# Performance work log

Measured on AMD Instinct MI355X. Metric: run time of the kernel, lower is better.

The kernel has to match this reference:

```python
import jax, jax.numpy as jnp
import numpy as np

B, K, T, H = 64, 49, 512, 512  # batch, regions, timesteps, hidden_size
A = 49                          # attention bottleneck dim (hard-coded in module)


def setup_inputs() -> dict:
    key = jax.random.key(0)
    ks = jax.random.split(key, 7)
    s = 1.0 / np.sqrt(H)
    return {
        "V":   jax.random.normal(ks[0], (B, K, H), jnp.float32),
        "h_t": jax.random.normal(ks[1], (B, T, H), jnp.float32),
        "s_t": jax.random.normal(ks[2], (B, T, H), jnp.float32),
        "Wv":  jax.random.normal(ks[3], (A, H), jnp.float32) * s,
        "Wg":  jax.random.normal(ks[4], (A, H), jnp.float32) * s,
        "Ws":  jax.random.normal(ks[5], (A, H), jnp.float32) * s,
        "Wh":  jax.random.normal(ks[6], (1, A), jnp.float32) * (1.0 / np.sqrt(A)),
    }


def reference(V, h_t, s_t, Wv, Wg, Ws, Wh):
    # Dropout is identity (eval mode). torch.nn.Linear: y = x @ W.T
    wh = Wh[0]                                     # [A]
    cv = jnp.einsum('bkh,ah->bka', V, Wv)          # [B,K,A]
    gh = jnp.einsum('bth,ah->bta', h_t, Wg)        # [B,T,A]
    content_v = cv[:, None, :, :] + gh[:, :, None, :]      # [B,T,K,A]
    z_t = jnp.einsum('btka,a->btk', jnp.tanh(content_v), wh)  # [B,T,K]
    alpha_t = jax.nn.softmax(z_t, axis=-1)         # softmax over K regions
    c_t = jnp.einsum('btk,bkh->bth', alpha_t, V)   # [B,T,H]

    content_s = jnp.einsum('bth,ah->bta', s_t, Ws) + gh       # [B,T,A]
    z_ext = jnp.einsum('bta,a->bt', jnp.tanh(content_s), wh)  # [B,T]
    extended = jnp.concatenate([z_t, z_ext[:, :, None]], axis=2)  # [B,T,K+1]
    alpha_hat = jax.nn.softmax(extended, axis=-1)
    beta_t = alpha_hat[:, :, -1:]                  # [B,T,1] sentinel gate

    c_hat_t = beta_t * s_t + (1.0 - beta_t) * c_t  # [B,T,H]
    return c_hat_t, alpha_t, beta_t
```

## Files before the change

kernel.cpp:

```cpp
#include <hip/hip_runtime.h>
#include <hip/hip_bf16.h>
#include <cstdint>
#include <cstddef>

#define NB 64
#define NK 49
#define NT 512
#define NH 512
#define NA 49

typedef __attribute__((ext_vector_type(8))) short bf16x8;
typedef __attribute__((ext_vector_type(4))) float f32x4;

__device__ __forceinline__ float fast_exp(float x) {
    return __builtin_amdgcn_exp2f(x * 1.4426950408889634f);
}
__device__ __forceinline__ float fast_tanh(float x) {
    float e = __builtin_amdgcn_exp2f(x * 2.8853900817779268f);
    return 1.0f - 2.0f * __builtin_amdgcn_rcpf(e + 1.0f);
}
__device__ __forceinline__ short bf16rn(float x) {
    unsigned b = __builtin_bit_cast(unsigned, x);
    unsigned r = b + 0x7FFFu + ((b >> 16) & 1u);
    return (short)(r >> 16);
}
__device__ __forceinline__ void split_hi_lo(float x, short& hi, short& lo) {
    unsigned b = __builtin_bit_cast(unsigned, x);
    unsigned hb = b & 0xFFFF0000u;
    hi = (short)(hb >> 16);
    lo = bf16rn(x - __builtin_bit_cast(float, hb));
}
__device__ __forceinline__ bf16x8 cvt8(float4 x0, float4 x1) {
    bf16x8 a;
    a[0] = bf16rn(x0.x); a[1] = bf16rn(x0.y); a[2] = bf16rn(x0.z); a[3] = bf16rn(x0.w);
    a[4] = bf16rn(x1.x); a[5] = bf16rn(x1.y); a[6] = bf16rn(x1.z); a[7] = bf16rn(x1.w);
    return a;
}

__global__ __launch_bounds__(256, 4) void kprew(
        const float* __restrict__ Wg, const float* __restrict__ Ws,
        const float* __restrict__ Wv, short* __restrict__ WB) {
    const int job = blockIdx.x >> 3, slice = blockIdx.x & 7;
    const float* W = (job == 0) ? Wg : (job == 1 ? Ws : Wv);
    short* dst = WB + (size_t)job * 65536;
    const int end = (slice + 1) * 8192;
    for (int idx = slice * 8192 + threadIdx.x; idx < end; idx += 256) {
        int e    = idx & 7;
        int lane = (idx >> 3) & 63;
        int ks   = (idx >> 9) & 15;
        int nt   = (idx >> 13) & 3;
        int sel  = idx >> 15;
        int a = nt * 16 + (lane & 15);
        int h = ks * 32 + (lane >> 4) * 8 + e;
        float x = (a < NA) ? W[a * NH + h] : 0.0f;
        short hi, lo; split_hi_lo(x, hi, lo);
        dst[idx] = sel ? lo : hi;
    }
}

__global__ __launch_bounds__(256, 4) void kprev(
        const float* __restrict__ V, const short* __restrict__ WB,
        short* __restrict__ VB, float* __restrict__ cv) {
    const int bid = blockIdx.x;
    if (bid < 512) {
        __shared__ float vl[NK * 64];
        const int b  = bid >> 3;
        const int sl = bid & 7;
        const int h0 = sl * 64;
        const float* Vb = V + (size_t)b * (NK * NH);
        for (int idx = threadIdx.x; idx < NK * 64; idx += 256) {
            int k = idx >> 6, c = idx & 63;
            vl[idx] = Vb[(size_t)k * NH + h0 + c];
        }
        __syncthreads();
        short* dst = VB + (size_t)b * 32768;
        for (int idx = threadIdx.x; idx < 4096; idx += 256) {
            int e    = idx & 7;
            int lane = (idx >> 3) & 63;
            int ks   = (idx >> 9) & 1;
            int ntl  = idx >> 10;
            int k = ks * 32 + (lane >> 4) * 8 + e;
            int c = ntl * 16 + (lane & 15);
            float x = (k < NK) ? vl[k * 64 + c] : 0.0f;
            dst[((size_t)(sl * 4 + ntl) * 2 + ks) * 512 + lane * 8 + e] = bf16rn(x);
        }
    } else {
        const int tid  = threadIdx.x;
        const int lane = tid & 63;
        const int w    = tid >> 6;
        const int m0   = (bid - 512) * 64 + w * 16;
        const int r    = lane & 15;
        const int g    = lane >> 4;

        const float* arow = V + (size_t)(m0 + r) * NH + g * 8;
        const bf16x8* wbv = (const bf16x8*)(WB + 2 * 65536);

        f32x4 acc0 = {0.f, 0.f, 0.f, 0.f};
        f32x4 acc1 = acc0, acc2 = acc0, acc3 = acc0;

        #pragma unroll 2
        for (int ks = 0; ks < 16; ++ks) {
            float4 x0 = *(const float4*)(arow + ks * 32);
            float4 x1 = *(const float4*)(arow + ks * 32 + 4);
            bf16x8 bh0 = wbv[(0 * 16 + ks) * 64 + lane];
            bf16x8 bh1 = wbv[(1 * 16 + ks) * 64 + lane];
            bf16x8 bh2 = wbv[(2 * 16 + ks) * 64 + lane];
            bf16x8 bh3 = wbv[(3 * 16 + ks) * 64 + lane];
            bf16x8 bl0 = wbv[(4 * 16 + ks) * 64 + lane];
            bf16x8 bl1 = wbv[(5 * 16 + ks) * 64 + lane];
            bf16x8 bl2 = wbv[(6 * 16 + ks) * 64 + lane];
            bf16x8 bl3 = wbv[(7 * 16 + ks) * 64 + lane];

            bf16x8 ahi, alo;
            {
                const float xs[8] = {x0.x, x0.y, x0.z, x0.w, x1.x, x1.y, x1.z, x1.w};
                #pragma unroll
                for (int e = 0; e < 8; ++e) { short hi, lo; split_hi_lo(xs[e], hi, lo); ahi[e] = hi; alo[e] = lo; }
            }
            acc0 = __builtin_amdgcn_mfma_f32_16x16x32_bf16(ahi, bh0, acc0, 0, 0, 0);
            acc0 = __builtin_amdgcn_mfma_f32_16x16x32_bf16(alo, bh0, acc0, 0, 0, 0);
            acc0 = __builtin_amdgcn_mfma_f32_16x16x32_bf16(ahi, bl0, acc0, 0, 0, 0);
            acc1 = __builtin_amdgcn_mfma_f32_16x16x32_bf16(ahi, bh1, acc1, 0, 0, 0);
            acc1 = __builtin_amdgcn_mfma_f32_16x16x32_bf16(alo, bh1, acc1, 0, 0, 0);
            acc1 = __builtin_amdgcn_mfma_f32_16x16x32_bf16(ahi, bl1, acc1, 0, 0, 0);
            acc2 = __builtin_amdgcn_mfma_f32_16x16x32_bf16(ahi, bh2, acc2, 0, 0, 0);
            acc2 = __builtin_amdgcn_mfma_f32_16x16x32_bf16(alo, bh2, acc2, 0, 0, 0);
            acc2 = __builtin_amdgcn_mfma_f32_16x16x32_bf16(ahi, bl2, acc2, 0, 0, 0);
            acc3 = __builtin_amdgcn_mfma_f32_16x16x32_bf16(ahi, bh3, acc3, 0, 0, 0);
            acc3 = __builtin_amdgcn_mfma_f32_16x16x32_bf16(alo, bh3, acc3, 0, 0, 0);
            acc3 = __builtin_amdgcn_mfma_f32_16x16x32_bf16(ahi, bl3, acc3, 0, 0, 0);
        }

        #pragma unroll
        for (int reg = 0; reg < 4; ++reg) {
            int row = m0 + g * 4 + reg;
            float* orow = cv + (size_t)row * 52;
            orow[ 0 + r] = acc0[reg];
            orow[16 + r] = acc1[reg];
            orow[32 + r] = acc2[reg];
            if (r == 0) orow[48] = acc3[reg];
        }
    }
}

__global__ __launch_bounds__(256, 4) void kfused(
        const float* __restrict__ h_t, const float* __restrict__ s_t,
        const float* __restrict__ Wh,
        const short* __restrict__ WB, const short* __restrict__ VB,
        const float* __restrict__ cv_ws,
        float* __restrict__ out_chat, float* __restrict__ out_alpha,
        float* __restrict__ out_beta) {
    __shared__ float cvl[NK * 52];
    __shared__ float ghl[32 * 52];
    __shared__ float ssl[32 * 52];
    __shared__ float zl[32 * 50];
    __shared__ short afrag[2048];
    __shared__ float whl[52];
    __shared__ float betal[32];

    const int tid  = threadIdx.x;
    const int lane = tid & 63;
    const int w    = tid >> 6;
    const int b    = blockIdx.x >> 4;
    const int t0   = (blockIdx.x & 15) * 32;
    const int r    = lane & 15;
    const int g    = lane >> 4;

    if (tid < NA) whl[tid] = Wh[tid];

    {
        const float* cvb = cv_ws + (size_t)b * (NK * 52);
        for (int idx = tid; idx < NK * 52; idx += 256) cvl[idx] = cvb[idx];
    }

    {
        const int job = w >> 1, mtile = w & 1;
        const float* in = job ? s_t : h_t;
        const bf16x8* wb = (const bf16x8*)(WB + (size_t)job * 65536);
        const float* arow = in + (size_t)(b * NT + t0 + mtile * 16 + r) * NH + g * 8;
        f32x4 acc0 = {0.f, 0.f, 0.f, 0.f};
        f32x4 acc1 = acc0, acc2 = acc0, acc3 = acc0;
        #pragma unroll 1
        for (int kp = 0; kp < 8; ++kp) {
            const int ksa = kp * 2, ksb = kp * 2 + 1;
            float4 xa0 = *(const float4*)(arow + ksa * 32);
            float4 xa1 = *(const float4*)(arow + ksa * 32 + 4);
            float4 xb0 = *(const float4*)(arow + ksb * 32);
            float4 xb1 = *(const float4*)(arow + ksb * 32 + 4);
            bf16x8 bh0a = wb[((0 + 0) * 16 + ksa) * 64 + lane];
            bf16x8 bh1a = wb[((0 + 1) * 16 + ksa) * 64 + lane];
            bf16x8 bh2a = wb[((0 + 2) * 16 + ksa) * 64 + lane];
            bf16x8 bh3a = wb[((0 + 3) * 16 + ksa) * 64 + lane];
            bf16x8 bl0a = wb[((4 + 0) * 16 + ksa) * 64 + lane];
            bf16x8 bl1a = wb[((4 + 1) * 16 + ksa) * 64 + lane];
            bf16x8 bl2a = wb[((4 + 2) * 16 + ksa) * 64 + lane];
            bf16x8 bl3a = wb[((4 + 3) * 16 + ksa) * 64 + lane];
            bf16x8 bh0b = wb[((0 + 0) * 16 + ksb) * 64 + lane];
            bf16x8 bh1b = wb[((0 + 1) * 16 + ksb) * 64 + lane];
            bf16x8 bh2b = wb[((0 + 2) * 16 + ksb) * 64 + lane];
            bf16x8 bh3b = wb[((0 + 3) * 16 + ksb) * 64 + lane];
            bf16x8 bl0b = wb[((4 + 0) * 16 + ksb) * 64 + lane];
            bf16x8 bl1b = wb[((4 + 1) * 16 + ksb) * 64 + lane];
            bf16x8 bl2b = wb[((4 + 2) * 16 + ksb) * 64 + lane];
            bf16x8 bl3b = wb[((4 + 3) * 16 + ksb) * 64 + lane];

            bf16x8 aa = cvt8(xa0, xa1);
            acc0 = __builtin_amdgcn_mfma_f32_16x16x32_bf16(aa, bh0a, acc0, 0, 0, 0);
            acc0 = __builtin_amdgcn_mfma_f32_16x16x32_bf16(aa, bl0a, acc0, 0, 0, 0);
            acc1 = __builtin_amdgcn_mfma_f32_16x16x32_bf16(aa, bh1a, acc1, 0, 0, 0);
            acc1 = __builtin_amdgcn_mfma_f32_16x16x32_bf16(aa, bl1a, acc1, 0, 0, 0);
            acc2 = __builtin_amdgcn_mfma_f32_16x16x32_bf16(aa, bh2a, acc2, 0, 0, 0);
            acc2 = __builtin_amdgcn_mfma_f32_16x16x32_bf16(aa, bl2a, acc2, 0, 0, 0);
            acc3 = __builtin_amdgcn_mfma_f32_16x16x32_bf16(aa, bh3a, acc3, 0, 0, 0);
            acc3 = __builtin_amdgcn_mfma_f32_16x16x32_bf16(aa, bl3a, acc3, 0, 0, 0);

            bf16x8 ab = cvt8(xb0, xb1);
            acc0 = __builtin_amdgcn_mfma_f32_16x16x32_bf16(ab, bh0b, acc0, 0, 0, 0);
            acc0 = __builtin_amdgcn_mfma_f32_16x16x32_bf16(ab, bl0b, acc0, 0, 0, 0);
            acc1 = __builtin_amdgcn_mfma_f32_16x16x32_bf16(ab, bh1b, acc1, 0, 0, 0);
            acc1 = __builtin_amdgcn_mfma_f32_16x16x32_bf16(ab, bl1b, acc1, 0, 0, 0);
            acc2 = __builtin_amdgcn_mfma_f32_16x16x32_bf16(ab, bh2b, acc2, 0, 0, 0);
            acc2 = __builtin_amdgcn_mfma_f32_16x16x32_bf16(ab, bl2b, acc2, 0, 0, 0);
            acc3 = __builtin_amdgcn_mfma_f32_16x16x32_bf16(ab, bh3b, acc3, 0, 0, 0);
            acc3 = __builtin_amdgcn_mfma_f32_16x16x32_bf16(ab, bl3b, acc3, 0, 0, 0);
        }
        float* dst = (w >> 1) ? ssl : ghl;
        #pragma unroll
        for (int reg = 0; reg < 4; ++reg) {
            int m = mtile * 16 + g * 4 + reg;
            dst[m * 52 +  0 + r] = acc0[reg];
            dst[m * 52 + 16 + r] = acc1[reg];
            dst[m * 52 + 32 + r] = acc2[reg];
            if (r < 4) dst[m * 52 + 48 + r] = acc3[reg];
        }
    }
    __syncthreads();

    {
        for (int p = tid; p < 32 * NK; p += 256) {
            int t = (int)(((unsigned)p * 1338u) >> 16);
            int k = p - t * NK;
            const float* rowp = cvl + k * 52;
            const float* gp   = ghl + t * 52;
            float zx = 0.f, zy = 0.f, zz = 0.f, zw = 0.f;
            #pragma unroll
            for (int q = 0; q < 12; ++q) {
                float4 rr = *(const float4*)(rowp + q * 4);
                float4 gg = *(const float4*)(gp + q * 4);
                zx = fmaf(whl[q * 4 + 0], fast_tanh(rr.x + gg.x), zx);
                zy = fmaf(whl[q * 4 + 1], fast_tanh(rr.y + gg.y), zy);
                zz = fmaf(whl[q * 4 + 2], fast_tanh(rr.z + gg.z), zz);
                zw = fmaf(whl[q * 4 + 3], fast_tanh(rr.w + gg.w), zw);
            }
            float z = (zx + zy) + (zz + zw);
            zl[t * 50 + k] = fmaf(whl[48], fast_tanh(rowp[48] + gp[48]), z);
        }
    }
    __syncthreads();

    {
        const int trow = w * 8 + (lane >> 3);
        const int sub  = lane & 7;
        float* zr = zl + trow * 50;

        float m = -1e30f;
        for (int k = sub; k < NK; k += 8) m = fmaxf(m, zr[k]);
        m = fmaxf(m, __shfl_xor(m, 1));
        m = fmaxf(m, __shfl_xor(m, 2));
        m = fmaxf(m, __shfl_xor(m, 4));

        float S = 0.0f;
        for (int k = sub; k < NK; k += 8) S += fast_exp(zr[k] - m);
        S += __shfl_xor(S, 1);
        S += __shfl_xor(S, 2);
        S += __shfl_xor(S, 4);
        float rS = __builtin_amdgcn_rcpf(S);

        const float* sp = ssl + trow * 52;
        const float* gp = ghl + trow * 52;
        float ze = 0.0f;
        for (int a = sub; a < NA; a += 8) ze = fmaf(whl[a], fast_tanh(sp[a] + gp[a]), ze);
        ze += __shfl_xor(ze, 1);
        ze += __shfl_xor(ze, 2);
        ze += __shfl_xor(ze, 4);

        float m50  = fmaxf(m, ze);
        float eext = fast_exp(ze - m50);
        float beta = eext * __builtin_amdgcn_rcpf(S * fast_exp(m - m50) + eext);
        if (sub == 0) {
            betal[trow] = beta;
            out_beta[(size_t)b * NT + t0 + trow] = beta;
        }

        const int mt = trow >> 4, rr2 = trow & 15;
        for (int k = sub; k < 64; k += 8) {
            float a = (k < NK) ? fast_exp(zr[k] - m) * rS : 0.0f;
            if (k < NK) zr[k] = a;
            int ks = k >> 5, gg = (k & 31) >> 3;
            afrag[(((ks * 2 + mt) * 64) + gg * 16 + rr2) * 8 + sub] = bf16rn(a);
        }
    }
    __syncthreads();

    {
        float* oa = out_alpha + ((size_t)b * NT + t0) * NK;
        for (int idx = tid; idx < 32 * NK; idx += 256) {
            int t = (int)(((unsigned)idx * 1338u) >> 16);
            int k = idx - t * NK;
            oa[idx] = zl[t * 50 + k];
        }
    }

    {
        const bf16x8* af = (const bf16x8*)afrag;
        const bf16x8* vb = (const bf16x8*)(VB + (size_t)b * 32768);
        const size_t rowb = (size_t)b * NT + t0;

        bf16x8 a00 = af[(0 * 2 + 0) * 64 + lane];
        bf16x8 a01 = af[(0 * 2 + 1) * 64 + lane];
        bf16x8 a10 = af[(1 * 2 + 0) * 64 + lane];
        bf16x8 a11 = af[(1 * 2 + 1) * 64 + lane];

        #pragma unroll 2
        for (int ntl = 0; ntl < 8; ++ntl) {
            const int nt = w * 8 + ntl;
            bf16x8 b0 = vb[(nt * 2 + 0) * 64 + lane];
            bf16x8 b1 = vb[(nt * 2 + 1) * 64 + lane];
            f32x4 acc0 = {0.f, 0.f, 0.f, 0.f};
            f32x4 acc1 = acc0;
            acc0 = __builtin_amdgcn_mfma_f32_16x16x32_bf16(a00, b0, acc0, 0, 0, 0);
            acc0 = __builtin_amdgcn_mfma_f32_16x16x32_bf16(a10, b1, acc0, 0, 0, 0);
            acc1 = __builtin_amdgcn_mfma_f32_16x16x32_bf16(a01, b0, acc1, 0, 0, 0);
            acc1 = __builtin_amdgcn_mfma_f32_16x16x32_bf16(a11, b1, acc1, 0, 0, 0);

            const int h0 = nt * 16 + r;
            #pragma unroll
            for (int reg = 0; reg < 4; ++reg) {
                {
                    int tloc = g * 4 + reg;
                    float bt = betal[tloc];
                    size_t off = (rowb + tloc) * NH + h0;
                    float s = s_t[off];
                    out_chat[off] = fmaf(bt, s - acc0[reg], acc0[reg]);
                }
                {
                    int tloc = 16 + g * 4 + reg;
                    float bt = betal[tloc];
                    size_t off = (rowb + tloc) * NH + h0;
                    float s = s_t[off];
                    out_chat[off] = fmaf(bt, s - acc1[reg], acc1[reg]);
                }
            }
        }
    }
}

extern "C" void kernel_launch(void* const* d_in, const int* in_sizes, int n_in,
                              void* d_out, int out_size, void* d_ws, size_t ws_size,
                              hipStream_t stream) {
    const float* V   = (const float*)d_in[0];
    const float* h_t = (const float*)d_in[1];
    const float* s_t = (const float*)d_in[2];
    const float* Wv  = (const float*)d_in[3];
    const float* Wg  = (const float*)d_in[4];
    const float* Ws  = (const float*)d_in[5];
    const float* Wh  = (const float*)d_in[6];

    float* out = (float*)d_out;
    float* out_chat  = out;
    float* out_alpha = out + (size_t)NB * NT * NH;
    float* out_beta  = out_alpha + (size_t)NB * NT * NK;

    short* WB = (short*)d_ws;
    short* VB = WB + (size_t)3 * 65536;
    float* cv = (float*)(VB + (size_t)64 * 32768);

    kprew<<<24, 256, 0, stream>>>(Wg, Ws, Wv, WB);
    kprev<<<561, 256, 0, stream>>>(V, WB, VB, cv);
    kfused<<<NB * 16, 256, 0, stream>>>(h_t, s_t, Wh, WB, VB, cv,
                                        out_chat, out_alpha, out_beta);
}
```

Measured before the change: 95.73 us.

## Halve fused kernel tile to 16 timesteps with 128 threads, read cv from global

The fused kernel now processes 16 timesteps per block with 2 waves instead of 32 timesteps with 4 waves, which doubles the grid and shrinks shared memory. The per-batch cv tile is no longer staged in LDS. Each thread reads its cv row straight from global/L2 into registers, with the tanh-sum loop unrolled by hand. The aim is higher occupancy and less LDS staging, at the cost of more redundant weight and cv reads across the larger number of blocks.

```diff
diff --git a/kernel.cpp b/kernel.cpp
--- a/kernel.cpp
+++ b/kernel.cpp
@@ -8,6 +8,7 @@
 #define NT 512
 #define NH 512
 #define NA 49
+#define TT 16
 
 typedef __attribute__((ext_vector_type(8))) short bf16x8;
 typedef __attribute__((ext_vector_type(4))) float f32x4;
@@ -143,41 +144,34 @@
     }
 }
 
-__global__ __launch_bounds__(256, 4) void kfused(
+__global__ __launch_bounds__(128, 4) void kfused(
         const float* __restrict__ h_t, const float* __restrict__ s_t,
         const float* __restrict__ Wh,
         const short* __restrict__ WB, const short* __restrict__ VB,
         const float* __restrict__ cv_ws,
         float* __restrict__ out_chat, float* __restrict__ out_alpha,
         float* __restrict__ out_beta) {
-    __shared__ float cvl[NK * 52];
-    __shared__ float ghl[32 * 52];
-    __shared__ float ssl[32 * 52];
-    __shared__ float zl[32 * 50];
-    __shared__ short afrag[2048];
+    __shared__ float ghl[TT * 52];
+    __shared__ float ssl[TT * 52];
+    __shared__ float zl[TT * 50];
+    __shared__ short afrag[1024];
     __shared__ float whl[52];
-    __shared__ float betal[32];
+    __shared__ float betal[TT];
 
     const int tid  = threadIdx.x;
     const int lane = tid & 63;
     const int w    = tid >> 6;
-    const int b    = blockIdx.x >> 4;
-    const int t0   = (blockIdx.x & 15) * 32;
+    const int b    = blockIdx.x >> 5;
+    const int t0   = (blockIdx.x & 31) * TT;
     const int r    = lane & 15;
     const int g    = lane >> 4;
 
     if (tid < NA) whl[tid] = Wh[tid];
 
     {
-        const float* cvb = cv_ws + (size_t)b * (NK * 52);
-        for (int idx = tid; idx < NK * 52; idx += 256) cvl[idx] = cvb[idx];
-    }
-
-    {
-        const int job = w >> 1, mtile = w & 1;
-        const float* in = job ? s_t : h_t;
-        const bf16x8* wb = (const bf16x8*)(WB + (size_t)job * 65536);
-        const float* arow = in + (size_t)(b * NT + t0 + mtile * 16 + r) * NH + g * 8;
+        const float* in = w ? s_t : h_t;
+        const bf16x8* wb = (const bf16x8*)(WB + (size_t)w * 65536);
+        const float* arow = in + (size_t)(b * NT + t0 + r) * NH + g * 8;
         f32x4 acc0 = {0.f, 0.f, 0.f, 0.f};
         f32x4 acc1 = acc0, acc2 = acc0, acc3 = acc0;
         #pragma unroll 1
@@ -224,10 +218,10 @@
             acc3 = __builtin_amdgcn_mfma_f32_16x16x32_bf16(ab, bh3b, acc3, 0, 0, 0);
             acc3 = __builtin_amdgcn_mfma_f32_16x16x32_bf16(ab, bl3b, acc3, 0, 0, 0);
         }
-        float* dst = (w >> 1) ? ssl : ghl;
+        float* dst = w ? ssl : ghl;
         #pragma unroll
         for (int reg = 0; reg < 4; ++reg) {
-            int m = mtile * 16 + g * 4 + reg;
+            int m = g * 4 + reg;
             dst[m * 52 +  0 + r] = acc0[reg];
             dst[m * 52 + 16 + r] = acc1[reg];
             dst[m * 52 + 32 + r] = acc2[reg];
@@ -237,23 +231,40 @@
     __syncthreads();
 
     {
-        for (int p = tid; p < 32 * NK; p += 256) {
+        const float* cvb = cv_ws + (size_t)b * (NK * 52);
+        for (int p = tid; p < TT * NK; p += 128) {
             int t = (int)(((unsigned)p * 1338u) >> 16);
             int k = p - t * NK;
-            const float* rowp = cvl + k * 52;
+            const float* rowp = cvb + (size_t)k * 52;
             const float* gp   = ghl + t * 52;
+            float4 rr0 = *(const float4*)(rowp +  0);
+            float4 rr1 = *(const float4*)(rowp +  4);
+            float4 rr2 = *(const float4*)(rowp +  8);
+            float4 rr3 = *(const float4*)(rowp + 12);
+            float4 rr4 = *(const float4*)(rowp + 16);
+            float4 rr5 = *(const float4*)(rowp + 20);
+            float4 rr6 = *(const float4*)(rowp + 24);
+            float4 rr7 = *(const float4*)(rowp + 28);
+            float4 rr8 = *(const float4*)(rowp + 32);
+            float4 rr9 = *(const float4*)(rowp + 36);
+            float4 rrA = *(const float4*)(rowp + 40);
+            float4 rrB = *(const float4*)(rowp + 44);
+            float r48  = rowp[48];
             float zx = 0.f, zy = 0.f, zz = 0.f, zw = 0.f;
-            #pragma unroll
-            for (int q = 0; q < 12; ++q) {
-                float4 rr = *(const float4*)(rowp + q * 4);
-                float4 gg = *(const float4*)(gp + q * 4);
-                zx = fmaf(whl[q * 4 + 0], fast_tanh(rr.x + gg.x), zx);
-                zy = fmaf(whl[q * 4 + 1], fast_tanh(rr.y + gg.y), zy);
-                zz = fmaf(whl[q * 4 + 2], fast_tanh(rr.z + gg.z), zz);
-                zw = fmaf(whl[q * 4 + 3], fast_tanh(rr.w + gg.w), zw);
-            }
+            const float4* gp4 = (const float4*)gp;
+            float4 gg;
+            #define ZSTEP(RR, Q) \
+                gg = gp4[Q]; \
+                zx = fmaf(whl[(Q)*4+0], fast_tanh(RR.x + gg.x), zx); \
+                zy = fmaf(whl[(Q)*4+1], fast_tanh(RR.y + gg.y), zy); \
+                zz = fmaf(whl[(Q)*4+2], fast_tanh(RR.z + gg.z), zz); \
+                zw = fmaf(whl[(Q)*4+3], fast_tanh(RR.w + gg.w), zw);
+            ZSTEP(rr0, 0)  ZSTEP(rr1, 1)  ZSTEP(rr2, 2)  ZSTEP(rr3, 3)
+            ZSTEP(rr4, 4)  ZSTEP(rr5, 5)  ZSTEP(rr6, 6)  ZSTEP(rr7, 7)
+            ZSTEP(rr8, 8)  ZSTEP(rr9, 9)  ZSTEP(rrA,10)  ZSTEP(rrB,11)
+            #undef ZSTEP
             float z = (zx + zy) + (zz + zw);
-            zl[t * 50 + k] = fmaf(whl[48], fast_tanh(rowp[48] + gp[48]), z);
+            zl[t * 50 + k] = fmaf(whl[48], fast_tanh(r48 + gp[48]), z);
         }
     }
     __syncthreads();
@@ -292,19 +303,18 @@
             out_beta[(size_t)b * NT + t0 + trow] = beta;
         }
 
-        const int mt = trow >> 4, rr2 = trow & 15;
         for (int k = sub; k < 64; k += 8) {
             float a = (k < NK) ? fast_exp(zr[k] - m) * rS : 0.0f;
             if (k < NK) zr[k] = a;
             int ks = k >> 5, gg = (k & 31) >> 3;
-            afrag[(((ks * 2 + mt) * 64) + gg * 16 + rr2) * 8 + sub] = bf16rn(a);
+            afrag[((ks * 64) + gg * 16 + trow) * 8 + sub] = bf16rn(a);
         }
     }
     __syncthreads();
 
     {
         float* oa = out_alpha + ((size_t)b * NT + t0) * NK;
-        for (int idx = tid; idx < 32 * NK; idx += 256) {
+        for (int idx = tid; idx < TT * NK; idx += 128) {
             int t = (int)(((unsigned)idx * 1338u) >> 16);
             int k = idx - t * NK;
             oa[idx] = zl[t * 50 + k];
@@ -316,40 +326,43 @@
         const bf16x8* vb = (const bf16x8*)(VB + (size_t)b * 32768);
         const size_t rowb = (size_t)b * NT + t0;
 
-        bf16x8 a00 = af[(0 * 2 + 0) * 64 + lane];
-        bf16x8 a01 = af[(0 * 2 + 1) * 64 + lane];
-        bf16x8 a10 = af[(1 * 2 + 0) * 64 + lane];
-        bf16x8 a11 = af[(1 * 2 + 1) * 64 + lane];
+        bf16x8 a0 = af[  0 + lane];
+        bf16x8 a1 = af[ 64 + lane];
+
+        const float bt0 = betal[g * 4 + 0];
+        const float bt1 = betal[g * 4 + 1];
+        const float bt2 = betal[g * 4 + 2];
+        const float bt3 = betal[g * 4 + 3];
 
         #pragma unroll 2
-        for (int ntl = 0; ntl < 8; ++ntl) {
-            const int nt = w * 8 + ntl;
+        for (int ntl = 0; ntl < 16; ++ntl) {
+            const int nt = w * 16 + ntl;
             bf16x8 b0 = vb[(nt * 2 + 0) * 64 + lane];
             bf16x8 b1 = vb[(nt * 2 + 1) * 64 + lane];
-            f32x4 acc0 = {0.f, 0.f, 0.f, 0.f};
-            f32x4 acc1 = acc0;
-            acc0 = __builtin_amdgcn_mfma_f32_16x16x32_bf16(a00, b0, acc0, 0, 0, 0);
-            acc0 = __builtin_amdgcn_mfma_f32_16x16x32_bf16(a10, b1, acc0, 0, 0, 0);
-            acc1 = __builtin_amdgcn_mfma_f32_16x16x32_bf16(a01, b0, acc1, 0, 0, 0);
-            acc1 = __builtin_amdgcn_mfma_f32_16x16x32_bf16(a11, b1, acc1, 0, 0, 0);
+            f32x4 acc = {0.f, 0.f, 0.f, 0.f};
+            acc = __builtin_amdgcn_mfma_f32_16x16x32_bf16(a0, b0, acc, 0, 0, 0);
+            acc = __builtin_amdgcn_mfma_f32_16x16x32_bf16(a1, b1, acc, 0, 0, 0);
 
             const int h0 = nt * 16 + r;
-            #pragma unroll
-            for (int reg = 0; reg < 4; ++reg) {
-                {
-                    int tloc = g * 4 + reg;
-                    float bt = betal[tloc];
-                    size_t off = (rowb + tloc) * NH + h0;
-                    float s = s_t[off];
-                    out_chat[off] = fmaf(bt, s - acc0[reg], acc0[reg]);
-                }
-                {
-                    int tloc = 16 + g * 4 + reg;
-                    float bt = betal[tloc];
-                    size_t off = (rowb + tloc) * NH + h0;
-                    float s = s_t[off];
-                    out_chat[off] = fmaf(bt, s - acc1[reg], acc1[reg]);
-                }
+            {
+                size_t off = (rowb + g * 4 + 0) * NH + h0;
+                float s = s_t[off];
+                out_chat[off] = fmaf(bt0, s - acc[0], acc[0]);
+            }
+            {
+                size_t off = (rowb + g * 4 + 1) * NH + h0;
+                float s = s_t[off];
+                out_chat[off] = fmaf(bt1, s - acc[1], acc[1]);
+            }
+            {
+                size_t off = (rowb + g * 4 + 2) * NH + h0;
+                float s = s_t[off];
+                out_chat[off] = fmaf(bt2, s - acc[2], acc[2]);
+            }
+            {
+                size_t off = (rowb + g * 4 + 3) * NH + h0;
+                float s = s_t[off];
+                out_chat[off] = fmaf(bt3, s - acc[3], acc[3]);
             }
         }
     }
@@ -377,6 +390,6 @@
 
     kprew<<<24, 256, 0, stream>>>(Wg, Ws, Wv, WB);
     kprev<<<561, 256, 0, stream>>>(V, WB, VB, cv);
-    kfused<<<NB * 16, 256, 0, stream>>>(h_t, s_t, Wh, WB, VB, cv,
-                                        out_chat, out_alpha, out_beta);
-}
+    kfused<<<NB * (NT / TT), 128, 0, stream>>>(h_t, s_t, Wh, WB, VB, cv,
+                                               out_chat, out_alpha, out_beta);
+}
```

Measured after the change: 112.7 us. 1.18x slower.

## Fuse score computation into softmax phase, prefetch cv into registers

Applied to the files above, without the earlier changes.

The cv tile is loaded as float4 into registers before the projection MFMAs and written to shared memory only afterwards, so its global latency overlaps the GEMM. The z-score loop is reassigned so each 8-lane group computes its own time row, with the running max folded in. This removes one block barrier and the separate max pass. Alpha is written straight to global from the softmax loop instead of through a shared-memory pass, which makes those stores more strided and less coalesced.

```diff
diff --git a/kernel.cpp b/kernel.cpp
--- a/kernel.cpp
+++ b/kernel.cpp
@@ -166,12 +166,13 @@
     const int r    = lane & 15;
     const int g    = lane >> 4;
 
+    const float4* cvb4 = (const float4*)(cv_ws + (size_t)b * (NK * 52));
+    const int ci0 = tid, ci1 = tid + 256, ci2 = tid + 512;
+    float4 cvr0 = cvb4[ci0 < 637 ? ci0 : 0];
+    float4 cvr1 = cvb4[ci1 < 637 ? ci1 : 0];
+    float4 cvr2 = cvb4[ci2 < 637 ? ci2 : 0];
+
     if (tid < NA) whl[tid] = Wh[tid];
-
-    {
-        const float* cvb = cv_ws + (size_t)b * (NK * 52);
-        for (int idx = tid; idx < NK * 52; idx += 256) cvl[idx] = cvb[idx];
-    }
 
     {
         const int job = w >> 1, mtile = w & 1;
@@ -234,14 +235,24 @@
             if (r < 4) dst[m * 52 + 48 + r] = acc3[reg];
         }
     }
+
+    {
+        float4* cvl4 = (float4*)cvl;
+        if (ci0 < 637) cvl4[ci0] = cvr0;
+        if (ci1 < 637) cvl4[ci1] = cvr1;
+        if (ci2 < 637) cvl4[ci2] = cvr2;
+    }
     __syncthreads();
 
     {
-        for (int p = tid; p < 32 * NK; p += 256) {
-            int t = (int)(((unsigned)p * 1338u) >> 16);
-            int k = p - t * NK;
+        const int trow = w * 8 + (lane >> 3);
+        const int sub  = lane & 7;
+        const float* gp = ghl + trow * 52;
+        float* zr = zl + trow * 50;
+
+        float m = -1e30f;
+        for (int k = sub; k < NK; k += 8) {
             const float* rowp = cvl + k * 52;
-            const float* gp   = ghl + t * 52;
             float zx = 0.f, zy = 0.f, zz = 0.f, zw = 0.f;
             #pragma unroll
             for (int q = 0; q < 12; ++q) {
@@ -253,18 +264,10 @@
                 zw = fmaf(whl[q * 4 + 3], fast_tanh(rr.w + gg.w), zw);
             }
             float z = (zx + zy) + (zz + zw);
-            zl[t * 50 + k] = fmaf(whl[48], fast_tanh(rowp[48] + gp[48]), z);
-        }
-    }
-    __syncthreads();
-
-    {
-        const int trow = w * 8 + (lane >> 3);
-        const int sub  = lane & 7;
-        float* zr = zl + trow * 50;
-
-        float m = -1e30f;
-        for (int k = sub; k < NK; k += 8) m = fmaxf(m, zr[k]);
+            z = fmaf(whl[48], fast_tanh(rowp[48] + gp[48]), z);
+            zr[k] = z;
+            m = fmaxf(m, z);
+        }
         m = fmaxf(m, __shfl_xor(m, 1));
         m = fmaxf(m, __shfl_xor(m, 2));
         m = fmaxf(m, __shfl_xor(m, 4));
@@ -277,7 +280,6 @@
         float rS = __builtin_amdgcn_rcpf(S);
 
         const float* sp = ssl + trow * 52;
-        const float* gp = ghl + trow * 52;
         float ze = 0.0f;
         for (int a = sub; a < NA; a += 8) ze = fmaf(whl[a], fast_tanh(sp[a] + gp[a]), ze);
         ze += __shfl_xor(ze, 1);
@@ -292,24 +294,19 @@
             out_beta[(size_t)b * NT + t0 + trow] = beta;
         }
 
+        float* oa = out_alpha + ((size_t)(b * NT + t0) + trow) * NK;
         const int mt = trow >> 4, rr2 = trow & 15;
         for (int k = sub; k < 64; k += 8) {
-            float a = (k < NK) ? fast_exp(zr[k] - m) * rS : 0.0f;
-            if (k < NK) zr[k] = a;
+            float a = 0.0f;
+            if (k < NK) {
+                a = fast_exp(zr[k] - m) * rS;
+                oa[k] = a;
+            }
             int ks = k >> 5, gg = (k & 31) >> 3;
             afrag[(((ks * 2 + mt) * 64) + gg * 16 + rr2) * 8 + sub] = bf16rn(a);
         }
     }
     __syncthreads();
-
-    {
-        float* oa = out_alpha + ((size_t)b * NT + t0) * NK;
-        for (int idx = tid; idx < 32 * NK; idx += 256) {
-            int t = (int)(((unsigned)idx * 1338u) >> 16);
-            int k = idx - t * NK;
-            oa[idx] = zl[t * 50 + k];
-        }
-    }
 
     {
         const bf16x8* af = (const bf16x8*)afrag;
```

New measurement: 154.3 us. 61.1% more time.
